# Optimization experiments

Hardware: AMD Instinct MI355X
Metric: run time of the kernel (lower is better)

Reference implementation:

```python
import jax, jax.numpy as jnp
import numpy as np

H, I, E, TOPK = 1024, 4096, 8, 2
B, S = 2, 2048


def setup_inputs() -> dict:
    key = jax.random.key(0)
    ks = jax.random.split(key, 6)
    x = jax.random.normal(ks[0], (B, S, H), dtype=jnp.float32)
    expert_indices = jax.random.randint(ks[1], (B, S, TOPK), 0, E)
    expert_weights = jax.random.uniform(ks[2], (B, S, TOPK), dtype=jnp.float32)
    gate_proj = jax.random.normal(ks[3], (E, I, H), dtype=jnp.float32) * 0.02
    up_proj = jax.random.normal(ks[4], (E, I, H), dtype=jnp.float32) * 0.02
    down_proj = jax.random.normal(ks[5], (E, H, I), dtype=jnp.float32) * 0.02
    return {"x": x, "expert_indices": expert_indices, "expert_weights": expert_weights,
            "gate_proj": gate_proj, "up_proj": up_proj, "down_proj": down_proj}


def reference(x, expert_indices, expert_weights, gate_proj, up_proj, down_proj):
    b, s, h = x.shape
    xf = x.reshape(-1, h)                      # [T, H]
    ei = expert_indices.reshape(-1, expert_indices.shape[-1])   # [T, K]
    ew = expert_weights.reshape(-1, expert_weights.shape[-1])   # [T, K]
    n_experts = gate_proj.shape[0]
    out = jnp.zeros_like(xf)
    for e in range(n_experts):
        # combined routing weight of this expert per token (sum over topk slots)
        w_e = jnp.sum(jnp.where(ei == e, ew, 0.0), axis=-1)     # [T]
        g = xf @ gate_proj[e].T                # [T, I]
        u = xf @ up_proj[e].T                  # [T, I]
        inter = jax.nn.silu(g) * u             # fused SiLU*mul
        out = out + w_e[:, None] * (inter @ down_proj[e].T)     # weighted scatter-add
    return out.reshape(b, s, h)
```

## Files before the change

kernel.cpp:

```cpp
#include <hip/hip_runtime.h>
#include <cstdint>
#include <cstddef>

#define H_DIM 1024
#define I_DIM 4096
#define E_NUM 8
#define TOPK  2
#define T_NUM 4096
#define NROWS (T_NUM * TOPK)
#define BK    32

typedef _Float16 half8 __attribute__((ext_vector_type(8)));
typedef float    f32x4 __attribute__((ext_vector_type(4)));

__device__ __forceinline__ void async_copy16(void* lds, const void* g)
{
    __builtin_amdgcn_global_load_lds(
        (__attribute__((address_space(1))) unsigned int*)g,
        (__attribute__((address_space(3))) unsigned int*)lds,
        16 , 0 , 0 );
}


#define NX4 (T_NUM * H_DIM / 4)
#define NW4 (E_NUM * I_DIM * H_DIM / 4)
__global__ void cvt_all(const float* __restrict__ x,  const float* __restrict__ gp,
                        const float* __restrict__ up, const float* __restrict__ dp,
                        _Float16* __restrict__ xh, _Float16* __restrict__ wg,
                        _Float16* __restrict__ wu, _Float16* __restrict__ wd)
{
    int i = blockIdx.x * blockDim.x + threadIdx.x;
    const int total = NX4 + 3 * NW4;
    if (i >= total) return;
    const float* s; _Float16* d; int j;
    if (i < NX4)              { s = x;  d = xh; j = i; }
    else if (i < NX4 + NW4)   { s = gp; d = wg; j = i - NX4; }
    else if (i < NX4 + 2*NW4) { s = up; d = wu; j = i - NX4 - NW4; }
    else                      { s = dp; d = wd; j = i - NX4 - 2*NW4; }
    float4 v = reinterpret_cast<const float4*>(s)[j];
    union { _Float16 h[4]; unsigned long long u; } o;
    o.h[0] = (_Float16)v.x; o.h[1] = (_Float16)v.y;
    o.h[2] = (_Float16)v.z; o.h[3] = (_Float16)v.w;
    reinterpret_cast<unsigned long long*>(d)[j] = o.u;
}

__global__ void route_all(const int* __restrict__ ei, const float* __restrict__ ew,
                          int* __restrict__ offs,
                          int* __restrict__ token_of_row, float* __restrict__ weight_of_row)
{
    __shared__ int cnt[E_NUM];
    __shared__ int cur[E_NUM];
    const int t = (int)threadIdx.x;
    if (t < E_NUM) cnt[t] = 0;
    __syncthreads();
    for (int s = t; s < NROWS; s += (int)blockDim.x) atomicAdd(&cnt[ei[s]], 1);
    __syncthreads();
    if (t == 0) {
        int acc = 0;
        for (int e = 0; e < E_NUM; ++e) { offs[e] = acc; cur[e] = acc; acc += cnt[e]; }
        offs[E_NUM] = acc;
    }
    __syncthreads();
    for (int s = t; s < NROWS; s += (int)blockDim.x) {
        int e = ei[s];
        int r = atomicAdd(&cur[e], 1);
        token_of_row[r]  = s >> 1;
        weight_of_row[r] = ew[s];
    }
}

__global__ __launch_bounds__(256) void gateup_gemm(
    const _Float16* __restrict__ xh,
    const _Float16* __restrict__ Wg,
    const _Float16* __restrict__ Wu,
    const int*      __restrict__ token_of_row,
    const int*      __restrict__ offs,
    _Float16*       __restrict__ inter)
{
    const int e = blockIdx.z;
    const int seg_start = offs[e], seg_end = offs[e + 1];
    const int m0 = seg_start + (int)blockIdx.y * 128;
    if (m0 >= seg_end) return;
    const int n0 = (int)blockIdx.x * 64;

    __shared__ _Float16 Ash[128 * BK];
    __shared__ _Float16 Bgs[64 * BK];
    __shared__ _Float16 Bus[64 * BK];

    const int tid  = (int)threadIdx.x;
    const int lane = tid & 63, wid = tid >> 6;
    const int wm = wid >> 1, wn = wid & 1;

    const int c   = lane & 3;
    const int rl  = lane >> 2;
    const int frl = (rl & 3) ^ (rl >> 2);
    const int gc  = c ^ frl;

    const _Float16* pA[2];
    _Float16* lA[2];
#pragma unroll
    for (int j = 0; j < 2; ++j) {
        int q = 2 * wid + j;
        int r = m0 + q * 16 + rl;
        if (r > seg_end - 1) r = seg_end - 1;
        int tok = token_of_row[r];
        pA[j] = xh + (size_t)tok * H_DIM + gc * 8;
        lA[j] = &Ash[q * 16 * BK];
    }
    const int brow = wid * 16 + rl;
    const _Float16* pBg = Wg + ((size_t)e * I_DIM + n0 + brow) * H_DIM + gc * 8;
    const _Float16* pBu = Wu + ((size_t)e * I_DIM + n0 + brow) * H_DIM + gc * 8;
    _Float16* lBg = &Bgs[wid * 16 * BK];
    _Float16* lBu = &Bus[wid * 16 * BK];

    f32x4 accg[4][2], accu[4][2];
#pragma unroll
    for (int i = 0; i < 4; ++i)
#pragma unroll
        for (int j = 0; j < 2; ++j) {
            accg[i][j] = (f32x4){0.f, 0.f, 0.f, 0.f};
            accu[i][j] = (f32x4){0.f, 0.f, 0.f, 0.f};
        }

    const int fm = lane & 15, kq = lane >> 4;
    const int fsw = (fm & 3) ^ ((fm >> 2) & 3);
    const int rdo = (kq ^ fsw) * 8;

    for (int kt = 0; kt < H_DIM / BK; ++kt) {
        const int ko = kt * BK;
        __syncthreads();
        async_copy16(lA[0], pA[0] + ko);
        async_copy16(lA[1], pA[1] + ko);
        async_copy16(lBg,   pBg   + ko);
        async_copy16(lBu,   pBu   + ko);
        __syncthreads();

        half8 a[4], bg[2], bu[2];
#pragma unroll
        for (int i = 0; i < 4; ++i)
            a[i] = *(const half8*)&Ash[(wm * 64 + i * 16 + fm) * BK + rdo];
#pragma unroll
        for (int j = 0; j < 2; ++j) {
            bg[j] = *(const half8*)&Bgs[(wn * 32 + j * 16 + fm) * BK + rdo];
            bu[j] = *(const half8*)&Bus[(wn * 32 + j * 16 + fm) * BK + rdo];
        }
#pragma unroll
        for (int i = 0; i < 4; ++i)
#pragma unroll
            for (int j = 0; j < 2; ++j) {
                accg[i][j] = __builtin_amdgcn_mfma_f32_16x16x32_f16(a[i], bg[j], accg[i][j], 0, 0, 0);
                accu[i][j] = __builtin_amdgcn_mfma_f32_16x16x32_f16(a[i], bu[j], accu[i][j], 0, 0, 0);
            }
    }

#pragma unroll
    for (int i = 0; i < 4; ++i) {
#pragma unroll
        for (int reg = 0; reg < 4; ++reg) {
            int r = m0 + wm * 64 + i * 16 + kq * 4 + reg;
            if (r < seg_end) {
#pragma unroll
                for (int j = 0; j < 2; ++j) {
                    int col = n0 + wn * 32 + j * 16 + fm;
                    float g = accg[i][j][reg];
                    float u = accu[i][j][reg];
                    float sv = (g / (1.f + __expf(-g))) * u;
                    inter[(size_t)r * I_DIM + col] = (_Float16)sv;
                }
            }
        }
    }
}

__global__ __launch_bounds__(256) void down_gemm(
    const _Float16* __restrict__ inter,
    const _Float16* __restrict__ Wd,
    const int*      __restrict__ token_of_row,
    const float*    __restrict__ weight_of_row,
    const int*      __restrict__ offs,
    float*          __restrict__ out)
{
    const int e = blockIdx.z;
    const int seg_start = offs[e], seg_end = offs[e + 1];
    const int m0 = seg_start + (int)blockIdx.y * 128;
    if (m0 >= seg_end) return;
    const int n0 = (int)blockIdx.x * 128;

    __shared__ _Float16 Ash[128 * BK];
    __shared__ _Float16 Bsh[128 * BK];

    const int tid  = (int)threadIdx.x;
    const int lane = tid & 63, wid = tid >> 6;
    const int wm = wid >> 1, wn = wid & 1;
    const int c   = lane & 3;
    const int rl  = lane >> 2;
    const int frl = (rl & 3) ^ (rl >> 2);
    const int gc  = c ^ frl;

    const _Float16* pA[2]; _Float16* lA[2];
    const _Float16* pB[2]; _Float16* lB[2];
#pragma unroll
    for (int j = 0; j < 2; ++j) {
        int q = 2 * wid + j;
        int row_in = q * 16 + rl;
        int r = m0 + row_in;
        if (r > seg_end - 1) r = seg_end - 1;
        pA[j] = inter + (size_t)r * I_DIM + gc * 8;
        lA[j] = &Ash[q * 16 * BK];
        int n = n0 + row_in;
        pB[j] = Wd + ((size_t)e * H_DIM + n) * I_DIM + gc * 8;
        lB[j] = &Bsh[q * 16 * BK];
    }

    f32x4 acc[4][4];
#pragma unroll
    for (int i = 0; i < 4; ++i)
#pragma unroll
        for (int j = 0; j < 4; ++j) acc[i][j] = (f32x4){0.f, 0.f, 0.f, 0.f};

    const int fm = lane & 15, kq = lane >> 4;
    const int fsw = (fm & 3) ^ ((fm >> 2) & 3);
    const int rdo = (kq ^ fsw) * 8;

    for (int kt = 0; kt < I_DIM / BK; ++kt) {
        const int ko = kt * BK;
        __syncthreads();
        async_copy16(lA[0], pA[0] + ko);
        async_copy16(lA[1], pA[1] + ko);
        async_copy16(lB[0], pB[0] + ko);
        async_copy16(lB[1], pB[1] + ko);
        __syncthreads();

        half8 a[4], b[4];
#pragma unroll
        for (int i = 0; i < 4; ++i)
            a[i] = *(const half8*)&Ash[(wm * 64 + i * 16 + fm) * BK + rdo];
#pragma unroll
        for (int j = 0; j < 4; ++j)
            b[j] = *(const half8*)&Bsh[(wn * 64 + j * 16 + fm) * BK + rdo];
#pragma unroll
        for (int i = 0; i < 4; ++i)
#pragma unroll
            for (int j = 0; j < 4; ++j)
                acc[i][j] = __builtin_amdgcn_mfma_f32_16x16x32_f16(a[i], b[j], acc[i][j], 0, 0, 0);
    }

#pragma unroll
    for (int i = 0; i < 4; ++i) {
#pragma unroll
        for (int reg = 0; reg < 4; ++reg) {
            int r = m0 + wm * 64 + i * 16 + kq * 4 + reg;
            if (r < seg_end) {
                float w = weight_of_row[r];
                int   t = token_of_row[r];
#pragma unroll
                for (int j = 0; j < 4; ++j) {
                    int col = n0 + wn * 64 + j * 16 + fm;
                    atomicAdd(&out[(size_t)t * H_DIM + col], w * acc[i][j][reg]);
                }
            }
        }
    }
}

extern "C" void kernel_launch(void* const* d_in, const int* in_sizes, int n_in,
                              void* d_out, int out_size, void* d_ws, size_t ws_size,
                              hipStream_t stream)
{
    const float* x  = (const float*)d_in[0];
    const int*   ei = (const int*)  d_in[1];
    const float* ew = (const float*)d_in[2];
    const float* gp = (const float*)d_in[3];
    const float* up = (const float*)d_in[4];
    const float* dp = (const float*)d_in[5];
    float* out = (float*)d_out;

    char* ws = (char*)d_ws;
    size_t o = 0;
    _Float16* xh    = (_Float16*)(ws + o); o += (size_t)T_NUM * H_DIM * 2;
    _Float16* Wg_h  = (_Float16*)(ws + o); o += (size_t)E_NUM * I_DIM * H_DIM * 2;
    _Float16* Wu_h  = (_Float16*)(ws + o); o += (size_t)E_NUM * I_DIM * H_DIM * 2;
    _Float16* Wd_h  = (_Float16*)(ws + o); o += (size_t)E_NUM * I_DIM * H_DIM * 2;
    _Float16* inter = (_Float16*)(ws + o); o += (size_t)NROWS * I_DIM * 2;
    int*   offs          = (int*)  (ws + o);
    int*   token_of_row  = (int*)  (ws + o + 256);
    float* weight_of_row = (float*)(ws + o + 256 + (size_t)NROWS * 4);
    size_t ws_need = o + 256 + (size_t)NROWS * 8;
    if (ws_size < ws_need) return;

    hipMemsetAsync(d_out, 0, (size_t)out_size * sizeof(float), stream);

    const int nt = 256;
    const int ncvt = NX4 + 3 * NW4;
    cvt_all<<<(ncvt + nt - 1) / nt, nt, 0, stream>>>(x, gp, up, dp, xh, Wg_h, Wu_h, Wd_h);

    route_all<<<1, 1024, 0, stream>>>(ei, ew, offs, token_of_row, weight_of_row);

    gateup_gemm<<<dim3(I_DIM / 64, NROWS / 128, E_NUM), 256, 0, stream>>>(
        xh, Wg_h, Wu_h, token_of_row, offs, inter);
    down_gemm<<<dim3(H_DIM / 128, NROWS / 128, E_NUM), 256, 0, stream>>>(
        inter, Wd_h, token_of_row, weight_of_row, offs, out);
}
```

Baseline: 713.1 us.

## Double-buffer LDS tiles in gate/up and down GEMMs to overlap loads with MFMA

Both expert GEMM kernels now keep two LDS buffers per operand and issue the async global-to-LDS copy for the next K-tile before computing on the current one. This halves the barriers per K step and aims to hide global load latency behind MFMA work. LDS use per block doubles, which may lower occupancy. Correctness depends on __syncthreads waiting for the async LDS loads.

```diff
diff --git a/kernel.cpp b/kernel.cpp
--- a/kernel.cpp
+++ b/kernel.cpp
@@ -83,9 +83,9 @@
     if (m0 >= seg_end) return;
     const int n0 = (int)blockIdx.x * 64;
 
-    __shared__ _Float16 Ash[128 * BK];
-    __shared__ _Float16 Bgs[64 * BK];
-    __shared__ _Float16 Bus[64 * BK];
+    __shared__ _Float16 Ash[2][128 * BK];
+    __shared__ _Float16 Bgs[2][64 * BK];
+    __shared__ _Float16 Bus[2][64 * BK];
 
     const int tid  = (int)threadIdx.x;
     const int lane = tid & 63, wid = tid >> 6;
@@ -97,7 +97,7 @@
     const int gc  = c ^ frl;
 
     const _Float16* pA[2];
-    _Float16* lA[2];
+    int offA[2];
 #pragma unroll
     for (int j = 0; j < 2; ++j) {
         int q = 2 * wid + j;
@@ -105,13 +105,12 @@
         if (r > seg_end - 1) r = seg_end - 1;
         int tok = token_of_row[r];
         pA[j] = xh + (size_t)tok * H_DIM + gc * 8;
-        lA[j] = &Ash[q * 16 * BK];
+        offA[j] = q * 16 * BK;
     }
     const int brow = wid * 16 + rl;
     const _Float16* pBg = Wg + ((size_t)e * I_DIM + n0 + brow) * H_DIM + gc * 8;
     const _Float16* pBu = Wu + ((size_t)e * I_DIM + n0 + brow) * H_DIM + gc * 8;
-    _Float16* lBg = &Bgs[wid * 16 * BK];
-    _Float16* lBu = &Bus[wid * 16 * BK];
+    const int offB = wid * 16 * BK;
 
     f32x4 accg[4][2], accu[4][2];
 #pragma unroll
@@ -126,23 +125,21 @@
     const int fsw = (fm & 3) ^ ((fm >> 2) & 3);
     const int rdo = (kq ^ fsw) * 8;
 
-    for (int kt = 0; kt < H_DIM / BK; ++kt) {
-        const int ko = kt * BK;
-        __syncthreads();
-        async_copy16(lA[0], pA[0] + ko);
-        async_copy16(lA[1], pA[1] + ko);
-        async_copy16(lBg,   pBg   + ko);
-        async_copy16(lBu,   pBu   + ko);
-        __syncthreads();
-
+    auto stage = [&](int buf, int ko) {
+        async_copy16(&Ash[buf][offA[0]], pA[0] + ko);
+        async_copy16(&Ash[buf][offA[1]], pA[1] + ko);
+        async_copy16(&Bgs[buf][offB],    pBg   + ko);
+        async_copy16(&Bus[buf][offB],    pBu   + ko);
+    };
+    auto compute = [&](int buf) {
         half8 a[4], bg[2], bu[2];
 #pragma unroll
         for (int i = 0; i < 4; ++i)
-            a[i] = *(const half8*)&Ash[(wm * 64 + i * 16 + fm) * BK + rdo];
+            a[i] = *(const half8*)&Ash[buf][(wm * 64 + i * 16 + fm) * BK + rdo];
 #pragma unroll
         for (int j = 0; j < 2; ++j) {
-            bg[j] = *(const half8*)&Bgs[(wn * 32 + j * 16 + fm) * BK + rdo];
-            bu[j] = *(const half8*)&Bus[(wn * 32 + j * 16 + fm) * BK + rdo];
+            bg[j] = *(const half8*)&Bgs[buf][(wn * 32 + j * 16 + fm) * BK + rdo];
+            bu[j] = *(const half8*)&Bus[buf][(wn * 32 + j * 16 + fm) * BK + rdo];
         }
 #pragma unroll
         for (int i = 0; i < 4; ++i)
@@ -151,6 +148,19 @@
                 accg[i][j] = __builtin_amdgcn_mfma_f32_16x16x32_f16(a[i], bg[j], accg[i][j], 0, 0, 0);
                 accu[i][j] = __builtin_amdgcn_mfma_f32_16x16x32_f16(a[i], bu[j], accu[i][j], 0, 0, 0);
             }
+    };
+
+    stage(0, 0);
+    __syncthreads();
+
+    constexpr int NK = H_DIM / BK;
+    for (int kt = 0; kt < NK; kt += 2) {
+        stage(1, (kt + 1) * BK);
+        compute(0);
+        __syncthreads();
+        if (kt + 2 < NK) stage(0, (kt + 2) * BK);
+        compute(1);
+        __syncthreads();
     }
 
 #pragma unroll
@@ -186,8 +196,8 @@
     if (m0 >= seg_end) return;
     const int n0 = (int)blockIdx.x * 128;
 
-    __shared__ _Float16 Ash[128 * BK];
-    __shared__ _Float16 Bsh[128 * BK];
+    __shared__ _Float16 Ash[2][128 * BK];
+    __shared__ _Float16 Bsh[2][128 * BK];
 
     const int tid  = (int)threadIdx.x;
     const int lane = tid & 63, wid = tid >> 6;
@@ -197,8 +207,8 @@
     const int frl = (rl & 3) ^ (rl >> 2);
     const int gc  = c ^ frl;
 
-    const _Float16* pA[2]; _Float16* lA[2];
-    const _Float16* pB[2]; _Float16* lB[2];
+    const _Float16* pA[2]; int offAB[2];
+    const _Float16* pB[2];
 #pragma unroll
     for (int j = 0; j < 2; ++j) {
         int q = 2 * wid + j;
@@ -206,10 +216,9 @@
         int r = m0 + row_in;
         if (r > seg_end - 1) r = seg_end - 1;
         pA[j] = inter + (size_t)r * I_DIM + gc * 8;
-        lA[j] = &Ash[q * 16 * BK];
+        offAB[j] = q * 16 * BK;
         int n = n0 + row_in;
         pB[j] = Wd + ((size_t)e * H_DIM + n) * I_DIM + gc * 8;
-        lB[j] = &Bsh[q * 16 * BK];
     }
 
     f32x4 acc[4][4];
@@ -222,27 +231,38 @@
     const int fsw = (fm & 3) ^ ((fm >> 2) & 3);
     const int rdo = (kq ^ fsw) * 8;
 
-    for (int kt = 0; kt < I_DIM / BK; ++kt) {
-        const int ko = kt * BK;
-        __syncthreads();
-        async_copy16(lA[0], pA[0] + ko);
-        async_copy16(lA[1], pA[1] + ko);
-        async_copy16(lB[0], pB[0] + ko);
-        async_copy16(lB[1], pB[1] + ko);
-        __syncthreads();
-
+    auto stage = [&](int buf, int ko) {
+        async_copy16(&Ash[buf][offAB[0]], pA[0] + ko);
+        async_copy16(&Ash[buf][offAB[1]], pA[1] + ko);
+        async_copy16(&Bsh[buf][offAB[0]], pB[0] + ko);
+        async_copy16(&Bsh[buf][offAB[1]], pB[1] + ko);
+    };
+    auto compute = [&](int buf) {
         half8 a[4], b[4];
 #pragma unroll
         for (int i = 0; i < 4; ++i)
-            a[i] = *(const half8*)&Ash[(wm * 64 + i * 16 + fm) * BK + rdo];
+            a[i] = *(const half8*)&Ash[buf][(wm * 64 + i * 16 + fm) * BK + rdo];
 #pragma unroll
         for (int j = 0; j < 4; ++j)
-            b[j] = *(const half8*)&Bsh[(wn * 64 + j * 16 + fm) * BK + rdo];
+            b[j] = *(const half8*)&Bsh[buf][(wn * 64 + j * 16 + fm) * BK + rdo];
 #pragma unroll
         for (int i = 0; i < 4; ++i)
 #pragma unroll
             for (int j = 0; j < 4; ++j)
                 acc[i][j] = __builtin_amdgcn_mfma_f32_16x16x32_f16(a[i], b[j], acc[i][j], 0, 0, 0);
+    };
+
+    stage(0, 0);
+    __syncthreads();
+
+    constexpr int NK = I_DIM / BK;
+    for (int kt = 0; kt < NK; kt += 2) {
+        stage(1, (kt + 1) * BK);
+        compute(0);
+        __syncthreads();
+        if (kt + 2 < NK) stage(0, (kt + 2) * BK);
+        compute(1);
+        __syncthreads();
     }
 
 #pragma unroll
```

Result: slower. 794.1 us (+11.4%).
